# Performance work log

Hardware: AMD Instinct MI355X
Metric: run time of the kernel (lower is better)

The kernel has to match this reference:

```python
import jax, jax.numpy as jnp
import numpy as np

D_HEAD = 64
D_MODEL = 1024
N_HEADS = D_MODEL // D_HEAD
MAX_TOKENS = 2048


def setup_inputs() -> dict:
    key = jax.random.key(0)
    ks = jax.random.split(key, 5)
    batch, pos = 2, 2048
    # kaiming_normal_ on (n_heads, d_model, d_head): fan_in = d_model*d_head -> std = sqrt(2/fan_in)
    std_qkv = np.sqrt(2.0 / (D_MODEL * D_HEAD)).astype(np.float32)
    # xavier_normal_ on (d_model, d_model): std = sqrt(2/(fan_in+fan_out))
    std_out = np.sqrt(2.0 / (D_MODEL + D_MODEL)).astype(np.float32)
    return {
        "residual_stream": jax.random.normal(ks[0], (batch, pos, D_MODEL), dtype=jnp.float32),
        "weight_query": jax.random.normal(ks[1], (N_HEADS, D_MODEL, D_HEAD), dtype=jnp.float32) * std_qkv,
        "weight_key": jax.random.normal(ks[2], (N_HEADS, D_MODEL, D_HEAD), dtype=jnp.float32) * std_qkv,
        "weight_value": jax.random.normal(ks[3], (N_HEADS, D_MODEL, D_HEAD), dtype=jnp.float32) * std_qkv,
        "weight_out": jax.random.normal(ks[4], (D_MODEL, D_MODEL), dtype=jnp.float32) * std_out,
    }


def reference(residual_stream, weight_query, weight_key, weight_value, weight_out):
    # QKV projections: [b, p, m] x [h, m, d] -> [b, h, p, d]
    q = jnp.einsum('bpm,hmd->bhpd', residual_stream, weight_query)
    k = jnp.einsum('bpm,hmd->bhpd', residual_stream, weight_key)
    v = jnp.einsum('bpm,hmd->bhpd', residual_stream, weight_value)

    n_tokens = residual_stream.shape[1]
    # scaled scores [b, h, dest, src]
    scores = jnp.einsum('bhqd,bhkd->bhqk', q, k) / jnp.sqrt(jnp.float32(D_HEAD))
    # causal mask: -inf above the diagonal
    causal = jnp.tril(jnp.ones((n_tokens, n_tokens), dtype=bool))
    scores = jnp.where(causal, scores, jnp.float32(-jnp.inf))
    pattern = jax.nn.softmax(scores, axis=-1)

    attn = jnp.einsum('bhqk,bhkd->bhqd', pattern, v)  # [b, h, dest, d_head]
    # concat heads -> [b, p, h*d_head]
    b, h, p, d = attn.shape
    attn_concat = jnp.transpose(attn, (0, 2, 1, 3)).reshape(b, p, h * d)
    return jnp.einsum('bpm,mn->bpn', attn_concat, weight_out)
```

## Files before the change

kernel.cpp:

```cpp
#include <hip/hip_runtime.h>
#include <hip/hip_bf16.h>
#include <stdint.h>


typedef __bf16 bf16x8 __attribute__((ext_vector_type(8)));
typedef float f32x4 __attribute__((ext_vector_type(4)));
typedef float f32x16 __attribute__((ext_vector_type(16)));
typedef unsigned short u16;

__device__ __forceinline__ u16 f2bf(float f) {
  unsigned u = __float_as_uint(f);
  u += 0x7fffu + ((u >> 16) & 1u);
  return (u16)(u >> 16);
}

__device__ __forceinline__ uint32_t cvtpk(float lo, float hi) {
  uint32_t r;
  asm("v_cvt_pk_bf16_f32 %0, %1, %2" : "=v"(r) : "v"(lo), "v"(hi));
  return r;
}

__device__ __forceinline__ void pl32swap(uint32_t& a, uint32_t& b) {
  asm volatile("v_permlane32_swap_b32 %0, %1" : "+v"(a), "+v"(b));
}

__device__ __forceinline__ float fexp2(float x) {
  float r;
  asm("v_exp_f32 %0, %1" : "=v"(r) : "v"(x));
  return r;
}

__device__ __forceinline__ void gload16(const u16* g, u16* l) {
  __builtin_amdgcn_global_load_lds(
      (__attribute__((address_space(1))) void*)(g),
      (__attribute__((address_space(3))) void*)(l), 16, 0, 0);
}

__global__ __launch_bounds__(256) void prep_k(const float* __restrict__ X,
                                              const float* __restrict__ Wq,
                                              const float* __restrict__ Wk,
                                              const float* __restrict__ Wv,
                                              const float* __restrict__ Wo,
                                              u16* __restrict__ Xb,
                                              u16* __restrict__ WqT,
                                              u16* __restrict__ WoT,
                                              int* __restrict__ flags) {
  __shared__ u16 tile[64][80];
  int bid = blockIdx.x, t = threadIdx.x;

  if (bid == 3072) {
    flags[t] = 0;
    return;
  }

  if (bid < 2048) {
    int i = (bid * 256 + t) * 8;
    float4 f0 = *reinterpret_cast<const float4*>(X + i);
    float4 f1 = *reinterpret_cast<const float4*>(X + i + 4);
    u16 tmp[8] = {f2bf(f0.x), f2bf(f0.y), f2bf(f0.z), f2bf(f0.w),
                  f2bf(f1.x), f2bf(f1.y), f2bf(f1.z), f2bf(f1.w)};
    *reinterpret_cast<uint4*>(Xb + i) = *reinterpret_cast<uint4*>(tmp);
    return;
  }

  if (bid < 2816) {
    int tq = bid - 2048;
    int rb = tq & 15, z = tq >> 4;
    int sel = z >> 4, head = z & 15;
    const float* W = (sel == 0) ? Wq : (sel == 1 ? Wk : Wv);
    const float* ip = W + (size_t)head * 65536;
    u16* op = WqT + (size_t)sel * 1048576 + (size_t)head * 65536;
    int r0 = rb * 64;
    int r = t >> 2, cb = (t & 3) * 16;
    const float4* src = reinterpret_cast<const float4*>(ip + (size_t)(r0 + r) * 64 + cb);
    u16 tmp[16];
#pragma unroll
    for (int v = 0; v < 4; v++) {
      float4 f = src[v];
      tmp[v * 4 + 0] = f2bf(f.x);
      tmp[v * 4 + 1] = f2bf(f.y);
      tmp[v * 4 + 2] = f2bf(f.z);
      tmp[v * 4 + 3] = f2bf(f.w);
    }
    *reinterpret_cast<uint4*>(&tile[r][cb]) = *reinterpret_cast<uint4*>(&tmp[0]);
    *reinterpret_cast<uint4*>(&tile[r][cb + 8]) = *reinterpret_cast<uint4*>(&tmp[8]);
    __syncthreads();
    int c = t >> 2, rbq = (t & 3) * 16;
    uint4 outv[2];
    u16* tp = reinterpret_cast<u16*>(outv);
#pragma unroll
    for (int j = 0; j < 16; j++) tp[j] = tile[rbq + j][c];
    uint4* dst = reinterpret_cast<uint4*>(op + (size_t)c * 1024 + r0 + rbq);
    dst[0] = outv[0];
    dst[1] = outv[1];
    return;
  }

  {
    int tc = bid - 2816;
    int r0 = (tc & 15) * 64;
    int c0 = (tc >> 4) * 64;
    int r = t >> 2, cb = (t & 3) * 16;
    const float4* src = reinterpret_cast<const float4*>(Wo + (size_t)(r0 + r) * 1024 + c0 + cb);
    u16 tmp[16];
#pragma unroll
    for (int v = 0; v < 4; v++) {
      float4 f = src[v];
      tmp[v * 4 + 0] = f2bf(f.x);
      tmp[v * 4 + 1] = f2bf(f.y);
      tmp[v * 4 + 2] = f2bf(f.z);
      tmp[v * 4 + 3] = f2bf(f.w);
    }
    *reinterpret_cast<uint4*>(&tile[r][cb]) = *reinterpret_cast<uint4*>(&tmp[0]);
    *reinterpret_cast<uint4*>(&tile[r][cb + 8]) = *reinterpret_cast<uint4*>(&tmp[8]);
    __syncthreads();
    int c = t >> 2, rbq = (t & 3) * 16;
    uint4 outv[2];
    u16* tp = reinterpret_cast<u16*>(outv);
#pragma unroll
    for (int j = 0; j < 16; j++) tp[j] = tile[rbq + j][c];
    uint4* dst = reinterpret_cast<uint4*>(WoT + (size_t)(c0 + c) * 1024 + r0 + rbq);
    dst[0] = outv[0];
    dst[1] = outv[1];
  }
}

__global__ __launch_bounds__(256) void qkv_gemm128_k(const u16* __restrict__ A,
                                                     const u16* __restrict__ BT,
                                                     u16* __restrict__ Q,
                                                     u16* __restrict__ K,
                                                     u16* __restrict__ VT2) {
  __shared__ __align__(16) u16 As[2][128][32];
  __shared__ __align__(16) u16 Bs[2][128][32];
  const float QSCALE = 0.125f * 1.44269504088896340736f;
  int m0 = blockIdx.x * 128, n0 = blockIdx.y * 128;
  int t = threadIdx.x, l = t & 63;
  int w = t >> 6, wm = w & 1, wn = w >> 1;
  int l15 = l & 15, q4 = l >> 4;
  int g = ((l & 3) - (l >> 3)) & 3;
  size_t lsrc = (size_t)(l >> 2) * 1024 + (size_t)(g * 8);
  const u16* ga = A + (size_t)(m0 + w * 32) * 1024 + lsrc;
  const u16* gb = BT + (size_t)(n0 + w * 32) * 1024 + lsrc;
  int rch = ((q4 + (l15 >> 1)) & 3) * 8;

  f32x4 acc[4][4];
  f32x4 z4 = {0.f, 0.f, 0.f, 0.f};
#pragma unroll
  for (int mi = 0; mi < 4; mi++)
#pragma unroll
    for (int nt = 0; nt < 4; nt++) acc[mi][nt] = z4;

  auto stage = [&](int buf, int k0) {
    gload16(ga + k0, &As[buf][w * 32][0]);
    gload16(ga + (size_t)16 * 1024 + k0, &As[buf][w * 32 + 16][0]);
    gload16(gb + k0, &Bs[buf][w * 32][0]);
    gload16(gb + (size_t)16 * 1024 + k0, &Bs[buf][w * 32 + 16][0]);
  };

  stage(0, 0);
  __syncthreads();

  for (int step = 0; step < 32; step++) {
    int cur = step & 1;
    if (step < 31) stage(cur ^ 1, (step + 1) * 32);
    bf16x8 af[4], bfr[4];
#pragma unroll
    for (int mi = 0; mi < 4; mi++)
      af[mi] = *reinterpret_cast<const bf16x8*>(&As[cur][wm * 64 + mi * 16 + l15][rch]);
#pragma unroll
    for (int nt = 0; nt < 4; nt++)
      bfr[nt] = *reinterpret_cast<const bf16x8*>(&Bs[cur][wn * 64 + nt * 16 + l15][rch]);
    __builtin_amdgcn_s_setprio(1);
#pragma unroll
    for (int mi = 0; mi < 4; mi++)
#pragma unroll
      for (int nt = 0; nt < 4; nt++)
        acc[mi][nt] = __builtin_amdgcn_mfma_f32_16x16x32_bf16(af[mi], bfr[nt], acc[mi][nt], 0, 0, 0);
    __builtin_amdgcn_s_setprio(0);
    __syncthreads();
  }

#pragma unroll
  for (int mi = 0; mi < 4; mi++) {
#pragma unroll
    for (int nt = 0; nt < 4; nt++) {
#pragma unroll
      for (int r = 0; r < 4; r++) {
        int m = m0 + wm * 64 + mi * 16 + q4 * 4 + r;
        int n = n0 + wn * 64 + nt * 16 + l15;
        int wsel = n >> 10, h = (n >> 6) & 15, d = n & 63;
        int b = m >> 11, p = m & 2047;
        size_t bh = (size_t)(b * 16 + h);
        float v = acc[mi][nt][r];
        if (wsel == 0)
          Q[(bh * 2048 + p) * 64 + d] = f2bf(v * QSCALE);
        else if (wsel == 1)
          K[(bh * 2048 + p) * 64 + d] = f2bf(v);
        else
          VT2[((bh * 32 + (p >> 6)) * 64 + d) * 64 + (p & 63)] = f2bf(v);
      }
    }
  }
}

__global__ __launch_bounds__(256) void out_gemm64_k(const u16* __restrict__ A,
                                                    const u16* __restrict__ BT,
                                                    float* __restrict__ O) {
  __shared__ __align__(16) u16 As[2][128][32];
  __shared__ __align__(16) u16 Bs[2][64][32];
  int m0 = blockIdx.x * 128, n0 = blockIdx.y * 64;
  int t = threadIdx.x, l = t & 63;
  int w = t >> 6, wm = w >> 1, wn = w & 1;
  int l15 = l & 15, q4 = l >> 4;
  int g = ((l & 3) - (l >> 3)) & 3;
  size_t lsrc = (size_t)(l >> 2) * 1024 + (size_t)(g * 8);
  const u16* ga = A + (size_t)(m0 + w * 32) * 1024 + lsrc;
  const u16* gb = BT + (size_t)(n0 + w * 16) * 1024 + lsrc;
  int rch = ((q4 + (l15 >> 1)) & 3) * 8;

  f32x4 acc[4][2];
  f32x4 z4 = {0.f, 0.f, 0.f, 0.f};
#pragma unroll
  for (int mi = 0; mi < 4; mi++)
#pragma unroll
    for (int nt = 0; nt < 2; nt++) acc[mi][nt] = z4;

  auto stage = [&](int buf, int k0) {
    gload16(ga + k0, &As[buf][w * 32][0]);
    gload16(ga + (size_t)16 * 1024 + k0, &As[buf][w * 32 + 16][0]);
    gload16(gb + k0, &Bs[buf][w * 16][0]);
  };

  stage(0, 0);
  __syncthreads();

  for (int step = 0; step < 32; step++) {
    int cur = step & 1;
    if (step < 31) stage(cur ^ 1, (step + 1) * 32);
    bf16x8 af[4], bfr[2];
#pragma unroll
    for (int mi = 0; mi < 4; mi++)
      af[mi] = *reinterpret_cast<const bf16x8*>(&As[cur][wm * 64 + mi * 16 + l15][rch]);
#pragma unroll
    for (int nt = 0; nt < 2; nt++)
      bfr[nt] = *reinterpret_cast<const bf16x8*>(&Bs[cur][wn * 32 + nt * 16 + l15][rch]);
    __builtin_amdgcn_s_setprio(1);
#pragma unroll
    for (int mi = 0; mi < 4; mi++)
#pragma unroll
      for (int nt = 0; nt < 2; nt++)
        acc[mi][nt] = __builtin_amdgcn_mfma_f32_16x16x32_bf16(af[mi], bfr[nt], acc[mi][nt], 0, 0, 0);
    __builtin_amdgcn_s_setprio(0);
    __syncthreads();
  }

#pragma unroll
  for (int mi = 0; mi < 4; mi++) {
#pragma unroll
    for (int nt = 0; nt < 2; nt++) {
#pragma unroll
      for (int r = 0; r < 4; r++) {
        int m = m0 + wm * 64 + mi * 16 + q4 * 4 + r;
        int n = n0 + wn * 32 + nt * 16 + l15;
        O[(size_t)m * 1024 + n] = acc[mi][nt][r];
      }
    }
  }
}

__global__ __launch_bounds__(256) void attn_k(const u16* __restrict__ Q,
                                              const u16* __restrict__ K,
                                              const u16* __restrict__ VT2,
                                              u16* __restrict__ A,
                                              float* __restrict__ Opart,
                                              int* __restrict__ flags) {
  __shared__ __align__(16) u16 Ks[2][64][64];
  __shared__ __align__(16) u16 Vs[2][64][64];
  int jx = blockIdx.x, h = blockIdx.y, b = blockIdx.z;
  int qt, ktA, ktB;
  bool wrHalf = false, cmHalf = false;
  if (jx < 8)       { qt = jx;      ktA = 0;      ktB = 2 * qt + 2; }
  else if (jx < 16) { qt = 23 - jx; ktA = 0;      ktB = qt + 1;  wrHalf = true; }
  else              { qt = 31 - jx; ktA = qt + 1; ktB = 2 * qt + 2; cmHalf = true; }
  size_t bh = (size_t)(b * 16 + h);
  int ps = (int)bh * 8 + (qt - 8);
  const u16* Qp = Q + bh * 2048 * 64;
  const u16* Kp = K + bh * 2048 * 64;
  const u16* Vt = VT2 + bh * 32 * 64 * 64;
  int t = threadIdx.x, l = t & 63, w = t >> 6;
  int l31 = l & 31, hi = l >> 5;
  int r8 = l >> 3, cs = ((l & 7) ^ r8) * 8;
  int swz = l31 & 7;
  const float NEG = -1e30f;
  const u16* kbase = Kp + (size_t)(w * 16 + r8) * 64 + cs;
  const u16* vbase = Vt + (size_t)(w * 16 + r8) * 64 + cs;
  int qrow = qt * 128 + w * 32 + l31;

  uint32_t onesw[4] = {0x3F803F80u, 0x3F803F80u, 0x3F803F80u, 0x3F803F80u};
  bf16x8 onesb = *reinterpret_cast<const bf16x8*>(onesw);

  bf16x8 qb[4];
#pragma unroll
  for (int kc = 0; kc < 4; kc++)
    qb[kc] = *reinterpret_cast<const bf16x8*>(Qp + (size_t)qrow * 64 + kc * 16 + hi * 8);

  f32x16 accO[2], rs_acc;
#pragma unroll
  for (int dh = 0; dh < 2; dh++)
#pragma unroll
    for (int r = 0; r < 16; r++) accO[dh][r] = 0.f;
#pragma unroll
  for (int r = 0; r < 16; r++) rs_acc[r] = 0.f;

#pragma unroll
  for (int j = 0; j < 2; j++) {
    gload16(kbase + (size_t)ktA * 4096 + j * 512, &Ks[ktA & 1][w * 16 + j * 8][0]);
    gload16(vbase + (size_t)ktA * 4096 + j * 512, &Vs[ktA & 1][w * 16 + j * 8][0]);
  }
  __syncthreads();

  for (int kt = ktA; kt < ktB; kt++) {
    int cur = kt & 1;
    if (kt < ktB - 1) {
      size_t off = (size_t)(kt + 1) * 4096;
#pragma unroll
      for (int j = 0; j < 2; j++) {
        gload16(kbase + off + j * 512, &Ks[cur ^ 1][w * 16 + j * 8][0]);
        gload16(vbase + off + j * 512, &Vs[cur ^ 1][w * 16 + j * 8][0]);
      }
    }

    f32x16 st[2];
#pragma unroll
    for (int kvh = 0; kvh < 2; kvh++)
#pragma unroll
      for (int r = 0; r < 16; r++) st[kvh][r] = 0.f;
    __builtin_amdgcn_s_setprio(1);
#pragma unroll
    for (int kc = 0; kc < 4; kc++) {
      bf16x8 ka0 = *reinterpret_cast<const bf16x8*>(
          &Ks[cur][l31][((2 * kc + hi) ^ swz) * 8]);
      bf16x8 ka1 = *reinterpret_cast<const bf16x8*>(
          &Ks[cur][32 + l31][((2 * kc + hi) ^ swz) * 8]);
      st[0] = __builtin_amdgcn_mfma_f32_32x32x16_bf16(ka0, qb[kc], st[0], 0, 0, 0);
      st[1] = __builtin_amdgcn_mfma_f32_32x32x16_bf16(ka1, qb[kc], st[1], 0, 0, 0);
    }
    __builtin_amdgcn_s_setprio(0);

    if (kt >= 2 * qt) {
      int kvb = kt * 64;
#pragma unroll
      for (int kvh = 0; kvh < 2; kvh++)
#pragma unroll
        for (int r = 0; r < 16; r++) {
          int kv = kvb + kvh * 32 + (r & 3) + 8 * (r >> 2) + 4 * hi;
          if (kv > qrow) st[kvh][r] = NEG;
        }
    }

#pragma unroll
    for (int kvh = 0; kvh < 2; kvh++)
#pragma unroll
      for (int r = 0; r < 16; r++) st[kvh][r] = fexp2(st[kvh][r]);

    bf16x8 pa[4];
#pragma unroll
    for (int ks = 0; ks < 4; ks++) {
      const f32x16& pp = st[ks >> 1];
      const int s8 = (ks & 1) * 8;
      uint32_t x0 = cvtpk(pp[s8 + 0], pp[s8 + 1]);
      uint32_t x1 = cvtpk(pp[s8 + 2], pp[s8 + 3]);
      uint32_t y0 = cvtpk(pp[s8 + 4], pp[s8 + 5]);
      uint32_t y1 = cvtpk(pp[s8 + 6], pp[s8 + 7]);
      pl32swap(x0, y0);
      pl32swap(x1, y1);
      uint32_t wds[4] = {x0, x1, y0, y1};
      pa[ks] = *reinterpret_cast<const bf16x8*>(wds);
    }

    __builtin_amdgcn_s_setprio(1);
#pragma unroll
    for (int ks = 0; ks < 4; ks++)
      rs_acc = __builtin_amdgcn_mfma_f32_32x32x16_bf16(pa[ks], onesb, rs_acc, 0, 0, 0);
#pragma unroll
    for (int dh = 0; dh < 2; dh++)
#pragma unroll
      for (int ks = 0; ks < 4; ks++) {
        bf16x8 vb = *reinterpret_cast<const bf16x8*>(
            &Vs[cur][dh * 32 + l31][((2 * ks + hi) ^ swz) * 8]);
        accO[dh] = __builtin_amdgcn_mfma_f32_32x32x16_bf16(pa[ks], vb, accO[dh], 0, 0, 0);
      }
    __builtin_amdgcn_s_setprio(0);
    __syncthreads();
  }

  if (wrHalf) {
    float* op = Opart + (size_t)ps * 12288;
#pragma unroll
    for (int i = 0; i < 16; i++) op[i * 256 + t] = accO[0][i];
#pragma unroll
    for (int i = 0; i < 16; i++) op[(16 + i) * 256 + t] = accO[1][i];
#pragma unroll
    for (int i = 0; i < 16; i++) op[(32 + i) * 256 + t] = rs_acc[i];
    __threadfence();
    __syncthreads();
    if (t == 0)
      __hip_atomic_store(&flags[ps], 1, __ATOMIC_RELEASE, __HIP_MEMORY_SCOPE_AGENT);
    return;
  }
  if (cmHalf) {
    if (t == 0) {
      while (__hip_atomic_load(&flags[ps], __ATOMIC_ACQUIRE, __HIP_MEMORY_SCOPE_AGENT) == 0)
        __builtin_amdgcn_s_sleep(8);
    }
    __syncthreads();
    const float* op = Opart + (size_t)ps * 12288;
#pragma unroll
    for (int i = 0; i < 16; i++) accO[0][i] += op[i * 256 + t];
#pragma unroll
    for (int i = 0; i < 16; i++) accO[1][i] += op[(16 + i) * 256 + t];
#pragma unroll
    for (int i = 0; i < 16; i++) rs_acc[i] += op[(32 + i) * 256 + t];
  }

#pragma unroll
  for (int r = 0; r < 16; r++) {
    float inv = 1.f / rs_acc[r];
    int ql = (r & 3) + 8 * (r >> 2) + 4 * hi;
    int prow = qt * 128 + w * 32 + ql;
    size_t base = ((size_t)(b * 2048 + prow)) * 1024 + h * 64;
    A[base + l31] = f2bf(accO[0][r] * inv);
    A[base + 32 + l31] = f2bf(accO[1][r] * inv);
  }
}

extern "C" void kernel_launch(void* const* d_in, const int* in_sizes, int n_in,
                              void* d_out, int out_size, void* d_ws, size_t ws_size,
                              hipStream_t stream) {
  const float* X  = (const float*)d_in[0];
  const float* Wq = (const float*)d_in[1];
  const float* Wk = (const float*)d_in[2];
  const float* Wv = (const float*)d_in[3];
  const float* Wo = (const float*)d_in[4];
  float* out = (float*)d_out;

  u16* ws = (u16*)d_ws;
  u16* WqT = ws;
  u16* WoT = WqT + 3145728;
  u16* Xb  = WoT + 1048576;
  u16* Qb  = Xb + 4194304;
  u16* Kb  = Qb + 4194304;
  u16* VT2 = Kb + 4194304;
  u16* Ab  = Xb;
  float* Opart = (float*)(VT2 + 4194304);
  int* flags = (int*)(Opart + 3145728);

  prep_k<<<dim3(3073), 256, 0, stream>>>(X, Wq, Wk, Wv, Wo, Xb, WqT, WoT, flags);
  qkv_gemm128_k<<<dim3(32, 24), 256, 0, stream>>>(Xb, WqT, Qb, Kb, VT2);
  attn_k<<<dim3(24, 16, 2), 256, 0, stream>>>(Qb, Kb, VT2, Ab, Opart, flags);
  out_gemm64_k<<<dim3(32, 16), 256, 0, stream>>>(Ab, WoT, out);
}
```

Measured before the change: 222.6 us.

## Replace split-KV flag handoff with triple-buffered KV pipeline and batch-reversed tile order

Removes the split of long causal query tiles across two blocks, along with the partial-sum buffer, the flag reset and the spin-wait handoff. Each block now handles a whole query tile. Blocks for batch 1 take tiles in reverse order so heavy and light tiles are interleaved for load balance. The K/V staging moves from double to triple buffering with explicit vmcnt waits and a single barrier per iteration, prefetching two tiles ahead. This adds LDS per block but drops the global partial round-trip and the cross-block sync. The trade-off is fewer blocks in flight and a longer critical path for the longest tiles.

```diff
diff --git a/kernel.cpp b/kernel.cpp
--- a/kernel.cpp
+++ b/kernel.cpp
@@ -43,15 +43,9 @@
                                               const float* __restrict__ Wo,
                                               u16* __restrict__ Xb,
                                               u16* __restrict__ WqT,
-                                              u16* __restrict__ WoT,
-                                              int* __restrict__ flags) {
+                                              u16* __restrict__ WoT) {
   __shared__ u16 tile[64][80];
   int bid = blockIdx.x, t = threadIdx.x;
-
-  if (bid == 3072) {
-    flags[t] = 0;
-    return;
-  }
 
   if (bid < 2048) {
     int i = (bid * 256 + t) * 8;
@@ -271,19 +265,12 @@
 __global__ __launch_bounds__(256) void attn_k(const u16* __restrict__ Q,
                                               const u16* __restrict__ K,
                                               const u16* __restrict__ VT2,
-                                              u16* __restrict__ A,
-                                              float* __restrict__ Opart,
-                                              int* __restrict__ flags) {
-  __shared__ __align__(16) u16 Ks[2][64][64];
-  __shared__ __align__(16) u16 Vs[2][64][64];
-  int jx = blockIdx.x, h = blockIdx.y, b = blockIdx.z;
-  int qt, ktA, ktB;
-  bool wrHalf = false, cmHalf = false;
-  if (jx < 8)       { qt = jx;      ktA = 0;      ktB = 2 * qt + 2; }
-  else if (jx < 16) { qt = 23 - jx; ktA = 0;      ktB = qt + 1;  wrHalf = true; }
-  else              { qt = 31 - jx; ktA = qt + 1; ktB = 2 * qt + 2; cmHalf = true; }
+                                              u16* __restrict__ A) {
+  __shared__ __align__(16) u16 Ks[3][64][64];
+  __shared__ __align__(16) u16 Vs[3][64][64];
+  int pr = blockIdx.x, h = blockIdx.y, b = blockIdx.z;
+  int qt = b ? (15 - pr) : pr;
   size_t bh = (size_t)(b * 16 + h);
-  int ps = (int)bh * 8 + (qt - 8);
   const u16* Qp = Q + bh * 2048 * 64;
   const u16* Kp = K + bh * 2048 * 64;
   const u16* Vt = VT2 + bh * 32 * 64 * 64;
@@ -292,6 +279,7 @@
   int r8 = l >> 3, cs = ((l & 7) ^ r8) * 8;
   int swz = l31 & 7;
   const float NEG = -1e30f;
+  int nkt = 2 * qt + 2;
   const u16* kbase = Kp + (size_t)(w * 16 + r8) * 64 + cs;
   const u16* vbase = Vt + (size_t)(w * 16 + r8) * 64 + cs;
   int qrow = qt * 128 + w * 32 + l31;
@@ -312,22 +300,29 @@
 #pragma unroll
   for (int r = 0; r < 16; r++) rs_acc[r] = 0.f;
 
-#pragma unroll
-  for (int j = 0; j < 2; j++) {
-    gload16(kbase + (size_t)ktA * 4096 + j * 512, &Ks[ktA & 1][w * 16 + j * 8][0]);
-    gload16(vbase + (size_t)ktA * 4096 + j * 512, &Vs[ktA & 1][w * 16 + j * 8][0]);
-  }
-  __syncthreads();
-
-  for (int kt = ktA; kt < ktB; kt++) {
-    int cur = kt & 1;
-    if (kt < ktB - 1) {
-      size_t off = (size_t)(kt + 1) * 4096;
-#pragma unroll
-      for (int j = 0; j < 2; j++) {
-        gload16(kbase + off + j * 512, &Ks[cur ^ 1][w * 16 + j * 8][0]);
-        gload16(vbase + off + j * 512, &Vs[cur ^ 1][w * 16 + j * 8][0]);
-      }
+  auto stageKV = [&](int buf, int kt) {
+    size_t off = (size_t)kt * 4096;
+#pragma unroll
+    for (int j = 0; j < 2; j++)
+      gload16(kbase + off + j * 512, &Ks[buf][w * 16 + j * 8][0]);
+#pragma unroll
+    for (int j = 0; j < 2; j++)
+      gload16(vbase + off + j * 512, &Vs[buf][w * 16 + j * 8][0]);
+  };
+
+  stageKV(0, 0);
+  stageKV(1, 1);
+
+  int cur = 0;
+  for (int kt = 0; kt < nkt; kt++) {
+    if (kt + 1 < nkt)
+      asm volatile("s_waitcnt vmcnt(4)" ::: "memory");
+    else
+      asm volatile("s_waitcnt vmcnt(0)" ::: "memory");
+    __builtin_amdgcn_s_barrier();
+    if (kt + 2 < nkt) {
+      int nb = cur + 2; if (nb >= 3) nb -= 3;
+      stageKV(nb, kt + 2);
     }
 
     f32x16 st[2];
@@ -391,36 +386,8 @@
         accO[dh] = __builtin_amdgcn_mfma_f32_32x32x16_bf16(pa[ks], vb, accO[dh], 0, 0, 0);
       }
     __builtin_amdgcn_s_setprio(0);
-    __syncthreads();
-  }
-
-  if (wrHalf) {
-    float* op = Opart + (size_t)ps * 12288;
-#pragma unroll
-    for (int i = 0; i < 16; i++) op[i * 256 + t] = accO[0][i];
-#pragma unroll
-    for (int i = 0; i < 16; i++) op[(16 + i) * 256 + t] = accO[1][i];
-#pragma unroll
-    for (int i = 0; i < 16; i++) op[(32 + i) * 256 + t] = rs_acc[i];
-    __threadfence();
-    __syncthreads();
-    if (t == 0)
-      __hip_atomic_store(&flags[ps], 1, __ATOMIC_RELEASE, __HIP_MEMORY_SCOPE_AGENT);
-    return;
-  }
-  if (cmHalf) {
-    if (t == 0) {
-      while (__hip_atomic_load(&flags[ps], __ATOMIC_ACQUIRE, __HIP_MEMORY_SCOPE_AGENT) == 0)
-        __builtin_amdgcn_s_sleep(8);
-    }
-    __syncthreads();
-    const float* op = Opart + (size_t)ps * 12288;
-#pragma unroll
-    for (int i = 0; i < 16; i++) accO[0][i] += op[i * 256 + t];
-#pragma unroll
-    for (int i = 0; i < 16; i++) accO[1][i] += op[(16 + i) * 256 + t];
-#pragma unroll
-    for (int i = 0; i < 16; i++) rs_acc[i] += op[(32 + i) * 256 + t];
+
+    cur = (cur == 2) ? 0 : cur + 1;
   }
 
 #pragma unroll
@@ -452,11 +419,9 @@
   u16* Kb  = Qb + 4194304;
   u16* VT2 = Kb + 4194304;
   u16* Ab  = Xb;
-  float* Opart = (float*)(VT2 + 4194304);
-  int* flags = (int*)(Opart + 3145728);
-
-  prep_k<<<dim3(3073), 256, 0, stream>>>(X, Wq, Wk, Wv, Wo, Xb, WqT, WoT, flags);
+
+  prep_k<<<dim3(3072), 256, 0, stream>>>(X, Wq, Wk, Wv, Wo, Xb, WqT, WoT);
   qkv_gemm128_k<<<dim3(32, 24), 256, 0, stream>>>(Xb, WqT, Qb, Kb, VT2);
-  attn_k<<<dim3(24, 16, 2), 256, 0, stream>>>(Qb, Kb, VT2, Ab, Opart, flags);
+  attn_k<<<dim3(16, 16, 2), 256, 0, stream>>>(Qb, Kb, VT2, Ab);
   out_gemm64_k<<<dim3(32, 16), 256, 0, stream>>>(Ab, WoT, out);
 }
```

Measured after the change: 187.7 us. -15.6%, faster.
